# Performance work log

Hardware: AMD Instinct MI355X
Metric: run time of the kernel (lower is better)

Reference implementation:

```python
import jax, jax.numpy as jnp
import numpy as np

B, IN, H = 8192, 1024, 1024

def setup_inputs() -> dict:
    key = jax.random.key(0)
    ks = jax.random.split(key, 12)
    s_i = 1.0 / np.sqrt(IN)   # lecun-normal-ish scale for input kernels
    s_h = 1.0 / np.sqrt(H)
    d = {
        'inputs': jax.random.normal(ks[0], (B, IN), jnp.float32),
        'c': jax.random.normal(ks[1], (B, H), jnp.float32),
        'h': jax.random.normal(ks[2], (B, H), jnp.float32),
    }
    for n, k in zip(['Wii', 'Wif', 'Wig', 'Wio'], ks[3:7]):
        d[n] = jax.random.normal(k, (IN, H), jnp.float32) * s_i
    for n, k in zip(['Whi', 'Whf', 'Whg', 'Who'], ks[7:11]):
        d[n] = jax.random.normal(k, (H, H), jnp.float32) * s_h
    for n in ['bi', 'bf', 'bg', 'bo']:
        d[n] = jnp.zeros((H,), jnp.float32)
    return d

def reference(inputs, c, h, Wii, Wif, Wig, Wio, Whi, Whf, Whg, Who, bi, bf, bg, bo):
    # i = sigmoid(x Wii + h Whi + bi); f, o likewise; g = tanh(x Wig + h Whg + bg)
    i = jax.nn.sigmoid(inputs @ Wii + h @ Whi + bi)
    f = jax.nn.sigmoid(inputs @ Wif + h @ Whf + bf)
    g = jnp.tanh(inputs @ Wig + h @ Whg + bg)
    o = jax.nn.sigmoid(inputs @ Wio + h @ Who + bo)
    new_c = f * c + i * g
    new_h = o * jnp.tanh(new_c)
    return (new_c, new_h)
```

## Files before the change

### kernel.cpp

```cpp
#include <hip/hip_runtime.h>
#include <hip/hip_bf16.h>
#include <cstdint>


#define B_DIM 8192
#define H_DIM 1024
#define K2    2048
#define N4    4096
#define BK    64
#define BM    256
#define BN    256
#define NT    (K2 / BK)

typedef __bf16 bf16x8 __attribute__((ext_vector_type(8)));
typedef float  f32x4  __attribute__((ext_vector_type(4)));

__device__ __forceinline__ void async_load16(const __bf16* g, __bf16* l) {
  __builtin_amdgcn_global_load_lds(
      (__attribute__((address_space(1))) void*)(g),
      (__attribute__((address_space(3))) void*)(l),
      16, 0, 0);
}

__device__ __forceinline__ float sigm(float x) {
  return 1.0f / (1.0f + __expf(-x));
}
__device__ __forceinline__ float tanh_fast(float x) {
  return 2.0f / (1.0f + __expf(-2.0f * x)) - 1.0f;
}

__global__ void cast_a(const float* __restrict__ x, const float* __restrict__ h,
                       __bf16* __restrict__ A) {
  const int r0 = blockIdx.x << 2;
  const int k = threadIdx.x << 3;
  const float* base;
  int koff;
  if (k < H_DIM) { base = x; koff = k; } else { base = h; koff = k - H_DIM; }
#pragma unroll
  for (int r = 0; r < 4; ++r) {
    const int row = r0 + r;
    const float* src = base + (size_t)row * H_DIM + koff;
    float4 v0 = *(const float4*)src;
    float4 v1 = *(const float4*)(src + 4);
    bf16x8 o;
    o[0] = (__bf16)v0.x; o[1] = (__bf16)v0.y; o[2] = (__bf16)v0.z; o[3] = (__bf16)v0.w;
    o[4] = (__bf16)v1.x; o[5] = (__bf16)v1.y; o[6] = (__bf16)v1.z; o[7] = (__bf16)v1.w;
    *(bf16x8*)&A[(size_t)row * K2 + k] = o;
  }
}

__global__ void cast_w(const float* __restrict__ Wii, const float* __restrict__ Wif,
                       const float* __restrict__ Wig, const float* __restrict__ Wio,
                       const float* __restrict__ Whi, const float* __restrict__ Whf,
                       const float* __restrict__ Whg, const float* __restrict__ Who,
                       __bf16* __restrict__ Bt) {
  __shared__ float tile[64][132];
  const int k0 = blockIdx.x * 64;
  const int j0 = blockIdx.y * 128;
  const int gate = blockIdx.z;
  const float* Wi[4] = {Wii, Wif, Wig, Wio};
  const float* Wh[4] = {Whi, Whf, Whg, Who};
  const float* W = (k0 < H_DIM) ? Wi[gate] : Wh[gate];
  const int kb = (k0 < H_DIM) ? k0 : (k0 - H_DIM);

  const int rr = threadIdx.x >> 3;
  const int cs = threadIdx.x & 7;
#pragma unroll
  for (int pass = 0; pass < 2; ++pass) {
    const int r = rr + pass * 32;
    const float* src = W + (size_t)(kb + r) * H_DIM + j0;
#pragma unroll
    for (int i = 0; i < 4; ++i) {
      float4 v = *(const float4*)(src + (cs + 8 * i) * 4);
      *(float4*)&tile[r][(cs + 8 * i) * 4] = v;
    }
  }
  __syncthreads();

  const int jl = threadIdx.x >> 1;
  const int kc = (threadIdx.x & 1) * 32;
  const int j  = j0 + jl;
  const int p  = ((j >> 4) << 6) + (gate << 4) + (j & 15);
  __bf16* dst = Bt + (size_t)p * K2 + k0 + kc;
#pragma unroll
  for (int cch = 0; cch < 4; ++cch) {
    bf16x8 o;
#pragma unroll
    for (int e = 0; e < 8; ++e) o[e] = (__bf16)tile[kc + cch * 8 + e][jl];
    *(bf16x8*)&dst[cch * 8] = o;
  }
}


#define STAGE_A(D, KH, TT) do { \
    async_load16(gA0 + (size_t)(TT) * 64 + (KH) * 32, &As_s[D][KH][wave << 9]); \
    async_load16(gA1 + (size_t)(TT) * 64 + (KH) * 32, &As_s[D][KH][4096 + (wave << 9)]); \
  } while (0)
#define STAGE_B(D, KH, TT) do { \
    async_load16(gB0 + (size_t)(TT) * 64 + (KH) * 32, &Bs_s[D][KH][wave << 9]); \
    async_load16(gB1 + (size_t)(TT) * 64 + (KH) * 32, &Bs_s[D][KH][4096 + (wave << 9)]); \
  } while (0)
#define STAGE_AB(D, KH, TT) do { STAGE_A(D, KH, TT); STAGE_B(D, KH, TT); } while (0)

#define DS_LOADS(DB, KK) do { \
    const __bf16* ap_ = &As_s[DB][KK][(wm << 12) + lane_part]; \
    const __bf16* bp_ = &Bs_s[DB][KK][(wn << 11) + lane_part]; \
    aF0[0] = *(const bf16x8*)(ap_);          aF0[1] = *(const bf16x8*)(ap_ + 512); \
    aF0[2] = *(const bf16x8*)(ap_ + 1024);   aF0[3] = *(const bf16x8*)(ap_ + 1536); \
    aF1[0] = *(const bf16x8*)(ap_ + 2048);   aF1[1] = *(const bf16x8*)(ap_ + 2560); \
    aF1[2] = *(const bf16x8*)(ap_ + 3072);   aF1[3] = *(const bf16x8*)(ap_ + 3584); \
    bF[0]  = *(const bf16x8*)(bp_);          bF[1]  = *(const bf16x8*)(bp_ + 512); \
    bF[2]  = *(const bf16x8*)(bp_ + 1024);   bF[3]  = *(const bf16x8*)(bp_ + 1536); \
  } while (0)

#define MFMA32() do { \
    __builtin_amdgcn_s_setprio(1); \
    _Pragma("unroll") \
    for (int i2 = 0; i2 < 4; ++i2) { \
      _Pragma("unroll") \
      for (int n2 = 0; n2 < 4; ++n2) \
        acc[i2][n2] = __builtin_amdgcn_mfma_f32_16x16x32_bf16( \
            aF0[i2], bF[n2], acc[i2][n2], 0, 0, 0); \
    } \
    _Pragma("unroll") \
    for (int i2 = 0; i2 < 4; ++i2) { \
      _Pragma("unroll") \
      for (int n2 = 0; n2 < 4; ++n2) \
        acc[4 + i2][n2] = __builtin_amdgcn_mfma_f32_16x16x32_bf16( \
            aF1[i2], bF[n2], acc[4 + i2][n2], 0, 0, 0); \
    } \
    __builtin_amdgcn_s_setprio(0); \
  } while (0)

#define GATE(N) asm volatile("s_waitcnt vmcnt(" #N ")" ::: "memory")

#define PHASE(DB, KK, STG, GT) do { \
    DS_LOADS(DB, KK); \
    STG; \
    MFMA32(); \
    GT; \
    __builtin_amdgcn_s_barrier(); \
  } while (0)

__global__ __launch_bounds__(512, 2) void lstm_gemm(
    const __bf16* __restrict__ A,
    const __bf16* __restrict__ Bt,
    const float* __restrict__ c,
    const float* __restrict__ bi, const float* __restrict__ bf_,
    const float* __restrict__ bg, const float* __restrict__ bo,
    float* __restrict__ out_c, float* __restrict__ out_h) {
  __shared__ __align__(16) __bf16 As_s[2][2][256 * 32];
  __shared__ __align__(16) __bf16 Bs_s[2][2][256 * 32];

  const int wg  = blockIdx.x;
  const int swz = ((wg & 7) << 6) + (wg >> 3);
  const int bx = swz & 31;
  const int by = swz >> 5;
  const int m0 = bx << 8;
  const int n0 = by << 8;

  const int tid  = threadIdx.x;
  const int wave = tid >> 6;
  const int lane = tid & 63;
  const int wm   = wave >> 2;
  const int wn   = wave & 3;

  const int srow = (wave << 4) + (lane >> 2);
  const int sgc  = (lane & 3) ^ ((lane >> 3) & 3);
  const __bf16* gA0 = A  + (size_t)(m0 + srow) * K2 + sgc * 8;
  const __bf16* gA1 = gA0 + (size_t)128 * K2;
  const __bf16* gB0 = Bt + (size_t)(n0 + srow) * K2 + sgc * 8;
  const __bf16* gB1 = gB0 + (size_t)128 * K2;

  const int lane_part = ((lane & 15) << 5) + ((((lane >> 4) ^ ((lane >> 1) & 3))) << 3);

  f32x4 acc[8][4] = {};
  bf16x8 aF0[4], aF1[4], bF[4];

  STAGE_AB(0, 0, 0);
  STAGE_AB(0, 1, 0);
  STAGE_AB(1, 0, 1);
  GATE(8);
  __builtin_amdgcn_s_barrier();

  for (int t = 0; t < NT - 2; t += 2) {
    PHASE(0, 0, STAGE_AB(1, 1, t + 1), GATE(8));
    PHASE(0, 1, STAGE_AB(0, 0, t + 2), GATE(8));
    PHASE(1, 0, STAGE_AB(0, 1, t + 2), GATE(8));
    PHASE(1, 1, STAGE_AB(1, 0, t + 3), GATE(8));
  }
  PHASE(0, 0, STAGE_AB(1, 1, NT - 1), GATE(8));
  PHASE(0, 1, (void)0, GATE(4));
  PHASE(1, 0, (void)0, GATE(0));
  DS_LOADS(1, 1);
  MFMA32();

  const int jj = (by << 6) + (wn << 4) + (lane & 15);
  const float vbi = bi[jj], vbf = bf_[jj], vbg = bg[jj], vbo = bo[jj];
  const int row_base = m0 + (wm << 7) + ((lane >> 4) << 2);
#pragma unroll
  for (int mi = 0; mi < 8; ++mi) {
#pragma unroll
    for (int r = 0; r < 4; ++r) {
      const int row = row_base + mi * 16 + r;
      const size_t idx = (size_t)row * H_DIM + jj;
      const float gi = sigm(acc[mi][0][r] + vbi);
      const float gf = sigm(acc[mi][1][r] + vbf);
      const float gg = tanh_fast(acc[mi][2][r] + vbg);
      const float go = sigm(acc[mi][3][r] + vbo);
      const float cv = c[idx];
      const float nc = gf * cv + gi * gg;
      out_c[idx] = nc;
      out_h[idx] = go * tanh_fast(nc);
    }
  }
}

extern "C" void kernel_launch(void* const* d_in, const int* in_sizes, int n_in,
                              void* d_out, int out_size, void* d_ws, size_t ws_size,
                              hipStream_t stream) {
  const float* x   = (const float*)d_in[0];
  const float* c   = (const float*)d_in[1];
  const float* h   = (const float*)d_in[2];
  const float* Wii = (const float*)d_in[3];
  const float* Wif = (const float*)d_in[4];
  const float* Wig = (const float*)d_in[5];
  const float* Wio = (const float*)d_in[6];
  const float* Whi = (const float*)d_in[7];
  const float* Whf = (const float*)d_in[8];
  const float* Whg = (const float*)d_in[9];
  const float* Who = (const float*)d_in[10];
  const float* bi  = (const float*)d_in[11];
  const float* bf_ = (const float*)d_in[12];
  const float* bg  = (const float*)d_in[13];
  const float* bo  = (const float*)d_in[14];

  __bf16* Abf = (__bf16*)d_ws;
  __bf16* Bt  = (__bf16*)((char*)d_ws + (size_t)B_DIM * K2 * 2);

  float* out_c = (float*)d_out;
  float* out_h = out_c + (size_t)B_DIM * H_DIM;

  cast_a<<<B_DIM / 4, 256, 0, stream>>>(x, h, Abf);
  dim3 gw(K2 / 64, H_DIM / 128, 4);
  cast_w<<<gw, 256, 0, stream>>>(Wii, Wif, Wig, Wio, Whi, Whf, Whg, Who, Bt);
  lstm_gemm<<<dim3((B_DIM / BM) * (N4 / BN)), 512, 0, stream>>>(
      Abf, Bt, c, bi, bf_, bg, bo, out_c, out_h);
}
```

Measured before the change: 335.4 us.

## Switch GEMM to 32x32x16 MFMA with 4x2 wave layout and c prefetch

Replaces the 16x16x32 MFMA tiling with 32x32x16 bf16 MFMA instructions, changes the wave grid from 2x4 to 4x2, and reworks the LDS fragment addressing. It also changes the weight packing to 32-column gate interleave, switches to a 2D XCD-aware block swizzle, and prefetches c before the last MFMA step. The cast kernels are simplified to smaller per-block work. The goal is fewer MFMA issues and LDS reads per FLOP plus better L2 locality, at the risk of more accumulator register pressure and different bank-conflict behaviour.

```diff
diff --git a/kernel.cpp b/kernel.cpp
--- a/kernel.cpp
+++ b/kernel.cpp
@@ -13,7 +13,7 @@
 #define NT    (K2 / BK)
 
 typedef __bf16 bf16x8 __attribute__((ext_vector_type(8)));
-typedef float  f32x4  __attribute__((ext_vector_type(4)));
+typedef float  f32x16 __attribute__((ext_vector_type(16)));
 
 __device__ __forceinline__ void async_load16(const __bf16* g, __bf16* l) {
   __builtin_amdgcn_global_load_lds(
@@ -31,22 +31,16 @@
 
 __global__ void cast_a(const float* __restrict__ x, const float* __restrict__ h,
                        __bf16* __restrict__ A) {
-  const int r0 = blockIdx.x << 2;
-  const int k = threadIdx.x << 3;
-  const float* base;
-  int koff;
-  if (k < H_DIM) { base = x; koff = k; } else { base = h; koff = k - H_DIM; }
-#pragma unroll
-  for (int r = 0; r < 4; ++r) {
-    const int row = r0 + r;
-    const float* src = base + (size_t)row * H_DIM + koff;
-    float4 v0 = *(const float4*)src;
-    float4 v1 = *(const float4*)(src + 4);
-    bf16x8 o;
-    o[0] = (__bf16)v0.x; o[1] = (__bf16)v0.y; o[2] = (__bf16)v0.z; o[3] = (__bf16)v0.w;
-    o[4] = (__bf16)v1.x; o[5] = (__bf16)v1.y; o[6] = (__bf16)v1.z; o[7] = (__bf16)v1.w;
-    *(bf16x8*)&A[(size_t)row * K2 + k] = o;
-  }
+  int row = blockIdx.x;
+  int k = threadIdx.x << 3;
+  const float* src = (k < H_DIM) ? (x + (size_t)row * H_DIM + k)
+                                 : (h + (size_t)row * H_DIM + (k - H_DIM));
+  float4 v0 = *(const float4*)src;
+  float4 v1 = *(const float4*)(src + 4);
+  bf16x8 o;
+  o[0] = (__bf16)v0.x; o[1] = (__bf16)v0.y; o[2] = (__bf16)v0.z; o[3] = (__bf16)v0.w;
+  o[4] = (__bf16)v1.x; o[5] = (__bf16)v1.y; o[6] = (__bf16)v1.z; o[7] = (__bf16)v1.w;
+  *(bf16x8*)&A[(size_t)row * K2 + k] = o;
 }
 
 __global__ void cast_w(const float* __restrict__ Wii, const float* __restrict__ Wif,
@@ -54,41 +48,30 @@
                        const float* __restrict__ Whi, const float* __restrict__ Whf,
                        const float* __restrict__ Whg, const float* __restrict__ Who,
                        __bf16* __restrict__ Bt) {
-  __shared__ float tile[64][132];
-  const int k0 = blockIdx.x * 64;
-  const int j0 = blockIdx.y * 128;
-  const int gate = blockIdx.z;
+  __shared__ float tile[64][33];
+  int k0 = blockIdx.x * 64;
+  int j0 = blockIdx.y * 32;
+  int gate = blockIdx.z;
   const float* Wi[4] = {Wii, Wif, Wig, Wio};
   const float* Wh[4] = {Whi, Whf, Whg, Who};
   const float* W = (k0 < H_DIM) ? Wi[gate] : Wh[gate];
-  const int kb = (k0 < H_DIM) ? k0 : (k0 - H_DIM);
-
-  const int rr = threadIdx.x >> 3;
-  const int cs = threadIdx.x & 7;
-#pragma unroll
-  for (int pass = 0; pass < 2; ++pass) {
-    const int r = rr + pass * 32;
-    const float* src = W + (size_t)(kb + r) * H_DIM + j0;
-#pragma unroll
-    for (int i = 0; i < 4; ++i) {
-      float4 v = *(const float4*)(src + (cs + 8 * i) * 4);
-      *(float4*)&tile[r][(cs + 8 * i) * 4] = v;
-    }
-  }
+  int kb = (k0 < H_DIM) ? k0 : (k0 - H_DIM);
+
+  int col = threadIdx.x & 31;
+  int rr  = threadIdx.x >> 5;
+#pragma unroll
+  for (int p = 0; p < 8; ++p)
+    tile[p * 8 + rr][col] = W[(size_t)(kb + p * 8 + rr) * H_DIM + j0 + col];
   __syncthreads();
 
-  const int jl = threadIdx.x >> 1;
-  const int kc = (threadIdx.x & 1) * 32;
-  const int j  = j0 + jl;
-  const int p  = ((j >> 4) << 6) + (gate << 4) + (j & 15);
-  __bf16* dst = Bt + (size_t)p * K2 + k0 + kc;
-#pragma unroll
-  for (int cch = 0; cch < 4; ++cch) {
-    bf16x8 o;
-#pragma unroll
-    for (int e = 0; e < 8; ++e) o[e] = (__bf16)tile[kc + cch * 8 + e][jl];
-    *(bf16x8*)&dst[cch * 8] = o;
-  }
+  int jj = threadIdx.x >> 3;
+  int ko = threadIdx.x & 7;
+  int j = j0 + jj;
+  int p = ((j >> 5) << 7) + (gate << 5) + (j & 31);
+  bf16x8 o;
+#pragma unroll
+  for (int t = 0; t < 8; ++t) o[t] = (__bf16)tile[ko * 8 + t][jj];
+  *(bf16x8*)&Bt[(size_t)p * K2 + k0 + ko * 8] = o;
 }
 
 
@@ -102,32 +85,28 @@
   } while (0)
 #define STAGE_AB(D, KH, TT) do { STAGE_A(D, KH, TT); STAGE_B(D, KH, TT); } while (0)
 
-#define DS_LOADS(DB, KK) do { \
-    const __bf16* ap_ = &As_s[DB][KK][(wm << 12) + lane_part]; \
-    const __bf16* bp_ = &Bs_s[DB][KK][(wn << 11) + lane_part]; \
-    aF0[0] = *(const bf16x8*)(ap_);          aF0[1] = *(const bf16x8*)(ap_ + 512); \
-    aF0[2] = *(const bf16x8*)(ap_ + 1024);   aF0[3] = *(const bf16x8*)(ap_ + 1536); \
-    aF1[0] = *(const bf16x8*)(ap_ + 2048);   aF1[1] = *(const bf16x8*)(ap_ + 2560); \
-    aF1[2] = *(const bf16x8*)(ap_ + 3072);   aF1[3] = *(const bf16x8*)(ap_ + 3584); \
-    bF[0]  = *(const bf16x8*)(bp_);          bF[1]  = *(const bf16x8*)(bp_ + 512); \
-    bF[2]  = *(const bf16x8*)(bp_ + 1024);   bF[3]  = *(const bf16x8*)(bp_ + 1536); \
-  } while (0)
-
-#define MFMA32() do { \
+#define DS_AB(DB, KK) do { \
+    const __bf16* ap_ = &As_s[DB][KK][a_off]; \
+    const __bf16* bp_ = &Bs_s[DB][KK][b_off]; \
+    aF[0][0] = *(const bf16x8*)(ap_ + o0);        aF[0][1] = *(const bf16x8*)(ap_ + o1); \
+    aF[1][0] = *(const bf16x8*)(ap_ + 1024 + o0); aF[1][1] = *(const bf16x8*)(ap_ + 1024 + o1); \
+    bF[0][0] = *(const bf16x8*)(bp_ + o0);        bF[0][1] = *(const bf16x8*)(bp_ + o1); \
+    bF[1][0] = *(const bf16x8*)(bp_ + 1024 + o0); bF[1][1] = *(const bf16x8*)(bp_ + 1024 + o1); \
+    bF[2][0] = *(const bf16x8*)(bp_ + 2048 + o0); bF[2][1] = *(const bf16x8*)(bp_ + 2048 + o1); \
+    bF[3][0] = *(const bf16x8*)(bp_ + 3072 + o0); bF[3][1] = *(const bf16x8*)(bp_ + 3072 + o1); \
+  } while (0)
+
+#define MFMA16() do { \
     __builtin_amdgcn_s_setprio(1); \
     _Pragma("unroll") \
-    for (int i2 = 0; i2 < 4; ++i2) { \
+    for (int tm = 0; tm < 2; ++tm) { \
       _Pragma("unroll") \
-      for (int n2 = 0; n2 < 4; ++n2) \
-        acc[i2][n2] = __builtin_amdgcn_mfma_f32_16x16x32_bf16( \
-            aF0[i2], bF[n2], acc[i2][n2], 0, 0, 0); \
-    } \
-    _Pragma("unroll") \
-    for (int i2 = 0; i2 < 4; ++i2) { \
-      _Pragma("unroll") \
-      for (int n2 = 0; n2 < 4; ++n2) \
-        acc[4 + i2][n2] = __builtin_amdgcn_mfma_f32_16x16x32_bf16( \
-            aF1[i2], bF[n2], acc[4 + i2][n2], 0, 0, 0); \
+      for (int tn = 0; tn < 4; ++tn) { \
+        acc[tm][tn] = __builtin_amdgcn_mfma_f32_32x32x16_bf16( \
+            aF[tm][0], bF[tn][0], acc[tm][tn], 0, 0, 0); \
+        acc[tm][tn] = __builtin_amdgcn_mfma_f32_32x32x16_bf16( \
+            aF[tm][1], bF[tn][1], acc[tm][tn], 0, 0, 0); \
+      } \
     } \
     __builtin_amdgcn_s_setprio(0); \
   } while (0)
@@ -135,9 +114,9 @@
 #define GATE(N) asm volatile("s_waitcnt vmcnt(" #N ")" ::: "memory")
 
 #define PHASE(DB, KK, STG, GT) do { \
-    DS_LOADS(DB, KK); \
+    DS_AB(DB, KK); \
     STG; \
-    MFMA32(); \
+    MFMA16(); \
     GT; \
     __builtin_amdgcn_s_barrier(); \
   } while (0)
@@ -153,17 +132,20 @@
   __shared__ __align__(16) __bf16 Bs_s[2][2][256 * 32];
 
   const int wg  = blockIdx.x;
-  const int swz = ((wg & 7) << 6) + (wg >> 3);
-  const int bx = swz & 31;
-  const int by = swz >> 5;
-  const int m0 = bx << 8;
-  const int n0 = by << 8;
+  const int xcd = wg & 7;
+  const int ii  = wg >> 3;
+  const int bx  = ((xcd & 3) << 3) + (ii & 7);
+  const int by  = ((xcd >> 2) << 3) + (ii >> 3);
+  const int m0  = bx << 8;
+  const int n0  = by << 8;
 
   const int tid  = threadIdx.x;
   const int wave = tid >> 6;
   const int lane = tid & 63;
-  const int wm   = wave >> 2;
-  const int wn   = wave & 3;
+  const int wm   = wave >> 1;
+  const int wn   = wave & 1;
+  const int lane31 = lane & 31;
+  const int h8   = lane >> 5;
 
   const int srow = (wave << 4) + (lane >> 2);
   const int sgc  = (lane & 3) ^ ((lane >> 3) & 3);
@@ -172,10 +154,14 @@
   const __bf16* gB0 = Bt + (size_t)(n0 + srow) * K2 + sgc * 8;
   const __bf16* gB1 = gB0 + (size_t)128 * K2;
 
-  const int lane_part = ((lane & 15) << 5) + ((((lane >> 4) ^ ((lane >> 1) & 3))) << 3);
-
-  f32x4 acc[8][4] = {};
-  bf16x8 aF0[4], aF1[4], bF[4];
+  const int swl = (lane31 >> 1) & 3;
+  const int o0  = (h8 ^ swl) << 3;
+  const int o1  = ((2 + h8) ^ swl) << 3;
+  const int a_off = (((wm << 6) + lane31) << 5);
+  const int b_off = (((wn << 7) + lane31) << 5);
+
+  f32x16 acc[2][4] = {};
+  bf16x8 aF[2][2], bF[4][2];
 
   STAGE_AB(0, 0, 0);
   STAGE_AB(0, 1, 0);
@@ -192,24 +178,31 @@
   PHASE(0, 0, STAGE_AB(1, 1, NT - 1), GATE(8));
   PHASE(0, 1, (void)0, GATE(4));
   PHASE(1, 0, (void)0, GATE(0));
-  DS_LOADS(1, 1);
-  MFMA32();
-
-  const int jj = (by << 6) + (wn << 4) + (lane & 15);
+
+  const int jj = (by << 6) + (wn << 5) + lane31;
+  const int rb = m0 + (wm << 6) + (h8 << 2);
+  float cpre[2][16];
+#pragma unroll
+  for (int tm = 0; tm < 2; ++tm)
+#pragma unroll
+    for (int r = 0; r < 16; ++r)
+      cpre[tm][r] = c[(size_t)(rb + tm * 32 + (r & 3) + 8 * (r >> 2)) * H_DIM + jj];
+
+  DS_AB(1, 1);
+  MFMA16();
+
   const float vbi = bi[jj], vbf = bf_[jj], vbg = bg[jj], vbo = bo[jj];
-  const int row_base = m0 + (wm << 7) + ((lane >> 4) << 2);
-#pragma unroll
-  for (int mi = 0; mi < 8; ++mi) {
-#pragma unroll
-    for (int r = 0; r < 4; ++r) {
-      const int row = row_base + mi * 16 + r;
+#pragma unroll
+  for (int tm = 0; tm < 2; ++tm) {
+#pragma unroll
+    for (int r = 0; r < 16; ++r) {
+      const int row = rb + tm * 32 + (r & 3) + 8 * (r >> 2);
       const size_t idx = (size_t)row * H_DIM + jj;
-      const float gi = sigm(acc[mi][0][r] + vbi);
-      const float gf = sigm(acc[mi][1][r] + vbf);
-      const float gg = tanh_fast(acc[mi][2][r] + vbg);
-      const float go = sigm(acc[mi][3][r] + vbo);
-      const float cv = c[idx];
-      const float nc = gf * cv + gi * gg;
+      const float gi = sigm(acc[tm][0][r] + vbi);
+      const float gf = sigm(acc[tm][1][r] + vbf);
+      const float gg = tanh_fast(acc[tm][2][r] + vbg);
+      const float go = sigm(acc[tm][3][r] + vbo);
+      const float nc = gf * cpre[tm][r] + gi * gg;
       out_c[idx] = nc;
       out_h[idx] = go * tanh_fast(nc);
     }
@@ -241,8 +234,8 @@
   float* out_c = (float*)d_out;
   float* out_h = out_c + (size_t)B_DIM * H_DIM;
 
-  cast_a<<<B_DIM / 4, 256, 0, stream>>>(x, h, Abf);
-  dim3 gw(K2 / 64, H_DIM / 128, 4);
+  cast_a<<<B_DIM, 256, 0, stream>>>(x, h, Abf);
+  dim3 gw(K2 / 64, H_DIM / 32, 4);
   cast_w<<<gw, 256, 0, stream>>>(Wii, Wif, Wig, Wio, Whi, Whf, Whg, Who, Bt);
   lstm_gemm<<<dim3((B_DIM / BM) * (N4 / BN)), 512, 0, stream>>>(
       Abf, Bt, c, bi, bf_, bg, bo, out_c, out_h);
```

Measured after the change: 368.3 us. +9.8%, slower.
